# Kernel tuning notes

Measured on AMD Instinct MI355X. Metric: run time of the kernel, lower is better.

The kernel has to match this reference:

```python
import jax, jax.numpy as jnp
import numpy as np

N = 20000      # nodes
E = 320000     # edges (avg degree 16)
IN = 512       # input feature dim
HID = 64       # hidden_dim
NH = 8         # n_heads
NC = 20        # n_classes
NG = 64        # graphs in batch
EPS = 1e-5     # batchnorm eps


def setup_inputs() -> dict:
    key = jax.random.key(0)
    ks = jax.random.split(key, 32)
    rn = lambda k, shape, s=0.05: (jax.random.normal(k, shape, jnp.float32) * s)
    inp = {
        "x": rn(ks[0], (N, IN), 1.0),
        "src": jax.random.randint(ks[1], (E,), 0, N),
        "dst": jax.random.randint(ks[2], (E,), 0, N),
        "graph_ids": jnp.sort(jax.random.randint(ks[3], (N,), 0, NG)),
        "n_graphs": NG,
        # encoder
        "W_enc": rn(ks[4], (IN, HID)), "b_enc": jnp.zeros((HID,), jnp.float32),
        # GAT layer 0
        "fc_W0": rn(ks[5], (HID, NH * HID)),
        "attn_l0": rn(ks[6], (NH, HID)), "attn_r0": rn(ks[7], (NH, HID)),
        "res_W0": rn(ks[8], (HID, NH * HID)),
        "bias0": jnp.zeros((NH * HID,), jnp.float32),
        "dp_W0": rn(ks[9], (NH * HID, HID)), "dp_b0": jnp.zeros((HID,), jnp.float32),
        # GAT layer 1
        "fc_W1": rn(ks[10], (HID, NH * HID)),
        "attn_l1": rn(ks[11], (NH, HID)), "attn_r1": rn(ks[12], (NH, HID)),
        "res_W1": rn(ks[13], (HID, NH * HID)),
        "bias1": jnp.zeros((NH * HID,), jnp.float32),
        "dp_W1": rn(ks[14], (NH * HID, HID)), "dp_b1": jnp.zeros((HID,), jnp.float32),
        # batchnorm affine
        "gamma": jnp.ones((2 * HID,), jnp.float32), "beta": jnp.zeros((2 * HID,), jnp.float32),
        # global attention pooling gate
        "gate_W": rn(ks[15], (2 * HID, 1)), "gate_b": jnp.zeros((1,), jnp.float32),
        # classifier
        "cls_W": rn(ks[16], (2 * HID, NC)), "cls_b": jnp.zeros((NC,), jnp.float32),
    }
    return inp


def gat_conv(h, fc_W, attn_l, attn_r, res_W, bias, src, dst, n_nodes):
    # DGL GATConv: fc -> per-head scalar scores -> edge softmax over incoming
    # edges -> weighted sum -> residual + bias -> leaky_relu activation.
    nh, d = attn_l.shape
    feat = (h @ fc_W).reshape(n_nodes, nh, d)              # [N,H,D]
    el = jnp.sum(feat * attn_l[None], axis=-1)             # [N,H]
    er = jnp.sum(feat * attn_r[None], axis=-1)             # [N,H]
    e = jax.nn.leaky_relu(el[src] + er[dst], 0.2)          # [E,H]
    m = jax.ops.segment_max(e, dst, num_segments=n_nodes)  # segment softmax
    ex = jnp.exp(e - m[dst])
    denom = jax.ops.segment_sum(ex, dst, num_segments=n_nodes)
    a = ex / denom[dst]                                    # [E,H]
    msg = feat[src] * a[:, :, None]                        # [E,H,D]  (dominant)
    rst = jax.ops.segment_sum(msg, dst, num_segments=n_nodes)  # [N,H,D]
    rst = rst + (h @ res_W).reshape(n_nodes, nh, d) + bias.reshape(nh, d)
    return jax.nn.leaky_relu(rst, 0.01)  # F.leaky_relu default slope


def reference(x, W_enc, b_enc,
              fc_W0, attn_l0, attn_r0, res_W0, bias0, dp_W0, dp_b0,
              fc_W1, attn_l1, attn_r1, res_W1, bias1, dp_W1, dp_b1,
              gamma, beta, gate_W, gate_b, cls_W, cls_b,
              src, dst, graph_ids, n_graphs):
    n_nodes = x.shape[0]
    he = x @ W_enc + b_enc                                  # encoder [N,HID]
    h = he
    h = gat_conv(h, fc_W0, attn_l0, attn_r0, res_W0, bias0, src, dst, n_nodes)
    h = h.reshape(n_nodes, -1) @ dp_W0 + dp_b0              # down_proj 0
    h = gat_conv(h, fc_W1, attn_l1, attn_r1, res_W1, bias1, src, dst, n_nodes)
    h = h.reshape(n_nodes, -1) @ dp_W1 + dp_b1              # down_proj 1
    hg = jnp.concatenate([h, he], axis=1)                   # [N,2*HID]
    # BatchNorm1d (training-mode batch stats, biased variance)
    mu = jnp.mean(hg, axis=0)
    var = jnp.var(hg, axis=0)
    hg = (hg - mu) * jax.lax.rsqrt(var + EPS) * gamma + beta
    # GlobalAttentionPooling: per-graph softmax over node gates
    gate = hg @ gate_W + gate_b                             # [N,1]
    gm = jax.ops.segment_max(gate, graph_ids, num_segments=n_graphs)
    ge = jnp.exp(gate - gm[graph_ids])
    gden = jax.ops.segment_sum(ge, graph_ids, num_segments=n_graphs)
    alpha = ge / gden[graph_ids]                            # [N,1]
    readout = jax.ops.segment_sum(alpha * hg, graph_ids, num_segments=n_graphs)
    return readout @ cls_W + cls_b                          # [NG,NC]
```

## Files before the change

### kernel.cpp

```cpp
#include <hip/hip_runtime.h>
#include <hip/hip_bf16.h>

#define MROWS   20000
#define N_EDGES 320000
#define DIN     512
#define HID     64
#define NH      8
#define ND      512
#define NCLS    20
#define NG      64
#define BN_EPS  1e-5f
#define PCH     16
#define BNB     256

typedef __hip_bfloat16 bf16;
typedef __attribute__((ext_vector_type(8))) short s16x8;
typedef __attribute__((ext_vector_type(4))) float f32x4;

enum { TF32 = 0, TBF16 = 1, TMODE = 2 };

__device__ __forceinline__ float ld_f32(const void* p, size_t i) { return ((const float*)p)[i]; }
__device__ __forceinline__ float ld_b16(const void* p, size_t i) { return __bfloat162float(((const bf16*)p)[i]); }

template<int T>
__device__ __forceinline__ float ldT(const void* p, size_t i, int bf) {
    if constexpr (T == TF32) return ld_f32(p, i);
    else if constexpr (T == TBF16) return ld_b16(p, i);
    else return bf ? ld_b16(p, i) : ld_f32(p, i);
}
template<int T>
__device__ __forceinline__ void stT(void* p, size_t i, int bf, float v) {
    if constexpr (T == TF32) ((float*)p)[i] = v;
    else if constexpr (T == TBF16) ((bf16*)p)[i] = __float2bfloat16(v);
    else { if (bf) ((bf16*)p)[i] = __float2bfloat16(v); else ((float*)p)[i] = v; }
}

__device__ __forceinline__ float bfbits2f(short s) {
    return __uint_as_float(((unsigned)(unsigned short)s) << 16);
}
__device__ __forceinline__ short f2bfbits(float v) {
    bf16 b = __float2bfloat16(v);
    return *reinterpret_cast<short*>(&b);
}

__global__ void detect_kernel(const void* __restrict__ gamma, int* __restrict__ mode) {
    if (threadIdx.x == 0 && blockIdx.x == 0)
        *mode = (*(const unsigned*)gamma == 0x3F800000u) ? 0 : 1;
}

struct TP { const void* src[7]; bf16* dst[7]; int K[7]; };
__global__ void transpose7_kernel(TP tp, const int* __restrict__ modep) {
    const int bf = *modep;
    int id = blockIdx.y;
    int i = blockIdx.x * 256 + threadIdx.x;
    int K = tp.K[id];
    int N = (DIN * HID) / K;
    int n = i / K, k = i - n * K;
    tp.dst[id][i] = __float2bfloat16(ldT<TMODE>(tp.src[id], (size_t)k * N + n, bf));
}

__global__ void convx_kernel(const void* __restrict__ x, bf16* __restrict__ xb,
                             const int* __restrict__ modep) {
    if (*modep) return;
    int i = (blockIdx.x * 256 + threadIdx.x) * 4;
    if (i >= MROWS * DIN) return;
    float4 v = ((const float4*)x)[i >> 2];
    xb[i + 0] = __float2bfloat16(v.x);
    xb[i + 1] = __float2bfloat16(v.y);
    xb[i + 2] = __float2bfloat16(v.z);
    xb[i + 3] = __float2bfloat16(v.w);
}

__global__ void hist_kernel(const int* __restrict__ keys, int* __restrict__ counts, int n) {
    int i = blockIdx.x * 256 + threadIdx.x;
    if (i < n) atomicAdd(&counts[keys[i]], 1);
}

__global__ void gsearch_kernel(const int* __restrict__ gids, int* __restrict__ goffs) {
    int g = threadIdx.x;
    if (g > NG) return;
    int lo = 0, hi = MROWS;
    while (lo < hi) {
        int mid = (lo + hi) >> 1;
        if (gids[mid] < g) lo = mid + 1; else hi = mid;
    }
    goffs[g] = lo;
}

__global__ __launch_bounds__(1024)
void scan1_kernel(const int* __restrict__ in, int* __restrict__ out,
                  int* __restrict__ partial, int n) {
    int i = blockIdx.x * 1024 + threadIdx.x;
    int v = (i < n) ? in[i] : 0;
    int lane = threadIdx.x & 63, wid = threadIdx.x >> 6;
    int s = v;
    #pragma unroll
    for (int o = 1; o < 64; o <<= 1) { int t = __shfl_up(s, o, 64); if (lane >= o) s += t; }
    __shared__ int wsum[16];
    if (lane == 63) wsum[wid] = s;
    __syncthreads();
    if (wid == 0 && lane < 16) {
        int t = wsum[lane];
        #pragma unroll
        for (int o = 1; o < 16; o <<= 1) { int u = __shfl_up(t, o, 64); if (lane >= o) t += u; }
        wsum[lane] = t;
    }
    __syncthreads();
    int carry = (wid > 0) ? wsum[wid - 1] : 0;
    int incl = s + carry;
    if (i < n) out[i] = incl - v;
    if (threadIdx.x == 1023) partial[blockIdx.x] = incl;
}

__global__ void scan2_kernel(int* __restrict__ partial, int nb) {
    int l = threadIdx.x;
    int v = (l < nb) ? partial[l] : 0;
    int s = v;
    #pragma unroll
    for (int o = 1; o < 64; o <<= 1) { int t = __shfl_up(s, o, 64); if (l >= o) s += t; }
    if (l < nb) partial[l] = s - v;
}

__global__ __launch_bounds__(1024)
void scan3_kernel(int* __restrict__ out, const int* __restrict__ partial, int n, int total) {
    int i = blockIdx.x * 1024 + threadIdx.x;
    if (i < n) out[i] += partial[blockIdx.x];
    if (i == 0) out[n] = total;
}

__global__ void scatter_kernel(const int* __restrict__ src, const int* __restrict__ dst,
                               const int* __restrict__ offs, int* __restrict__ cursor,
                               int* __restrict__ src_sorted) {
    int e = blockIdx.x * 256 + threadIdx.x;
    if (e < N_EDGES) {
        int d = dst[e];
        int pos = offs[d] + atomicAdd(&cursor[d], 1);
        src_sorted[pos] = src[e];
    }
}

template<int K, int NB, int NTOT>
__global__ __launch_bounds__(256)
void gemm_mfma(const void* __restrict__ Araw, const bf16* __restrict__ Aconv,
               const bf16* __restrict__ BT, const void* __restrict__ bias,
               bf16* __restrict__ C, const int* __restrict__ modep) {
    const int bf = *modep;
    const bf16* A = bf ? (const bf16*)Araw : Aconv;
    const int wid  = threadIdx.x >> 6;
    const int lane = threadIdx.x & 63;
    const int quad = lane >> 4;
    const int l16  = lane & 15;
    const int rb = blockIdx.x * 128 + wid * 32;
    const int cb = blockIdx.y * NB;
    constexpr int CT = NB / 16;
    constexpr int KC = K / 32;

    f32x4 acc[2][CT] = {};
    int r0 = rb + l16;       if (r0 >= MROWS) r0 = MROWS - 1;
    int r1 = rb + 16 + l16;  if (r1 >= MROWS) r1 = MROWS - 1;
    const bf16* a0p = A + (size_t)r0 * K + quad * 8;
    const bf16* a1p = A + (size_t)r1 * K + quad * 8;
    const bf16* btp = BT + (size_t)(cb + l16) * K + quad * 8;

    for (int kc = 0; kc < KC; ++kc) {
        s16x8 af0 = *(const s16x8*)(a0p + kc * 32);
        s16x8 af1 = *(const s16x8*)(a1p + kc * 32);
        s16x8 bfr[CT];
        #pragma unroll
        for (int ct = 0; ct < CT; ++ct)
            bfr[ct] = *(const s16x8*)(btp + (size_t)ct * 16 * K + kc * 32);
        #pragma unroll
        for (int ct = 0; ct < CT; ++ct) {
            acc[0][ct] = __builtin_amdgcn_mfma_f32_16x16x32_bf16(af0, bfr[ct], acc[0][ct], 0, 0, 0);
            acc[1][ct] = __builtin_amdgcn_mfma_f32_16x16x32_bf16(af1, bfr[ct], acc[1][ct], 0, 0, 0);
        }
    }
    #pragma unroll
    for (int ct = 0; ct < CT; ++ct) {
        int col = cb + ct * 16 + l16;
        float bb = bias ? ldT<TMODE>(bias, col, bf) : 0.f;
        #pragma unroll
        for (int rt = 0; rt < 2; ++rt) {
            #pragma unroll
            for (int rg = 0; rg < 4; ++rg) {
                int row = rb + rt * 16 + quad * 4 + rg;
                if (row < MROWS)
                    C[(size_t)row * NTOT + col] = __float2bfloat16(acc[rt][ct][rg] + bb);
            }
        }
    }
}

__global__ __launch_bounds__(256)
void gemm_fcres(const bf16* __restrict__ A, const bf16* __restrict__ BT_fc,
                const bf16* __restrict__ BT_res, const void* __restrict__ bias,
                const void* __restrict__ attn_l, const void* __restrict__ attn_r,
                bf16* __restrict__ feat, bf16* __restrict__ rst,
                float* __restrict__ el, float* __restrict__ er,
                const int* __restrict__ modep) {
    const int bf = *modep;
    const bool isres = blockIdx.y >= 4;
    const int yy = blockIdx.y & 3;
    const bf16* BT = isres ? BT_res : BT_fc;
    bf16* C = isres ? rst : feat;
    const int wid  = threadIdx.x >> 6;
    const int lane = threadIdx.x & 63;
    const int quad = lane >> 4;
    const int l16  = lane & 15;
    const int rb = blockIdx.x * 128 + wid * 32;
    const int cb = yy * 128;
    constexpr int CT = 8;
    constexpr int K  = HID;
    constexpr int KC = K / 32;

    f32x4 acc[2][CT] = {};
    int r0 = rb + l16;       if (r0 >= MROWS) r0 = MROWS - 1;
    int r1 = rb + 16 + l16;  if (r1 >= MROWS) r1 = MROWS - 1;
    const bf16* a0p = A + (size_t)r0 * K + quad * 8;
    const bf16* a1p = A + (size_t)r1 * K + quad * 8;
    const bf16* btp = BT + (size_t)(cb + l16) * K + quad * 8;

    #pragma unroll
    for (int kc = 0; kc < KC; ++kc) {
        s16x8 af0 = *(const s16x8*)(a0p + kc * 32);
        s16x8 af1 = *(const s16x8*)(a1p + kc * 32);
        s16x8 bfr[CT];
        #pragma unroll
        for (int ct = 0; ct < CT; ++ct)
            bfr[ct] = *(const s16x8*)(btp + (size_t)ct * 16 * K + kc * 32);
        #pragma unroll
        for (int ct = 0; ct < CT; ++ct) {
            acc[0][ct] = __builtin_amdgcn_mfma_f32_16x16x32_bf16(af0, bfr[ct], acc[0][ct], 0, 0, 0);
            acc[1][ct] = __builtin_amdgcn_mfma_f32_16x16x32_bf16(af1, bfr[ct], acc[1][ct], 0, 0, 0);
        }
    }
    #pragma unroll
    for (int ct = 0; ct < CT; ++ct) {
        int col = cb + ct * 16 + l16;
        float bb = isres ? ldT<TMODE>(bias, col, bf) : 0.f;
        #pragma unroll
        for (int rt = 0; rt < 2; ++rt) {
            #pragma unroll
            for (int rg = 0; rg < 4; ++rg) {
                int row = rb + rt * 16 + quad * 4 + rg;
                if (row < MROWS)
                    C[(size_t)row * ND + col] = __float2bfloat16(acc[rt][ct][rg] + bb);
            }
        }
    }
    if (!isres) {
        float al[CT], ar[CT];
        #pragma unroll
        for (int ct = 0; ct < CT; ++ct) {
            int col = cb + ct * 16 + l16;
            al[ct] = ldT<TMODE>(attn_l, col, bf);
            ar[ct] = ldT<TMODE>(attn_r, col, bf);
        }
        #pragma unroll
        for (int rt = 0; rt < 2; ++rt) {
            #pragma unroll
            for (int rg = 0; rg < 4; ++rg) {
                float e0 = 0.f, e1 = 0.f, f0 = 0.f, f1 = 0.f;
                #pragma unroll
                for (int ct = 0; ct < 4; ++ct) {
                    e0 += acc[rt][ct][rg] * al[ct];
                    f0 += acc[rt][ct][rg] * ar[ct];
                    e1 += acc[rt][ct + 4][rg] * al[ct + 4];
                    f1 += acc[rt][ct + 4][rg] * ar[ct + 4];
                }
                #pragma unroll
                for (int o = 1; o < 16; o <<= 1) {
                    e0 += __shfl_xor(e0, o, 64);
                    e1 += __shfl_xor(e1, o, 64);
                    f0 += __shfl_xor(f0, o, 64);
                    f1 += __shfl_xor(f1, o, 64);
                }
                int row = rb + rt * 16 + quad * 4 + rg;
                if (row < MROWS) {
                    if (l16 == 0) { el[row * 8 + 2 * yy] = e0;     er[row * 8 + 2 * yy] = f0; }
                    if (l16 == 1) { el[row * 8 + 2 * yy + 1] = e1; er[row * 8 + 2 * yy + 1] = f1; }
                }
            }
        }
    }
}

__global__ __launch_bounds__(256)
void agg_kernel(const bf16* __restrict__ feat, const float* __restrict__ el,
                const float* __restrict__ er, const int* __restrict__ offs,
                const int* __restrict__ srcs, bf16* __restrict__ rst) {
    int gid = blockIdx.x * 256 + threadIdx.x;
    int n = gid >> 6;
    int l = threadIdx.x & 63;
    if (n >= MROWS) return;
    int hh = l >> 3;
    int e0 = __builtin_amdgcn_readfirstlane(offs[n]);
    int e1 = __builtin_amdgcn_readfirstlane(offs[n + 1]);
    float er_h = er[n * 8 + hh];
    float acc[8] = {0.f, 0.f, 0.f, 0.f, 0.f, 0.f, 0.f, 0.f};
    float den = 0.f;
    for (int base = e0; base < e1; base += 64) {
        int cnt = min(64, e1 - base);
        int sv = (base + l < e1) ? srcs[base + l] : 0;
        for (int eb = 0; eb < cnt; eb += 8) {
            int en = cnt - eb;
            s16x8 ff[8];
            float elv[8];
            int lastv = cnt - 1;
            #pragma unroll
            for (int p = 0; p < 8; ++p) {
                int idx = eb + p; if (idx > lastv) idx = lastv;
                int s = __shfl(sv, idx, 64);
                ff[p] = *(const s16x8*)(feat + (size_t)s * ND + l * 8);
                elv[p] = el[s * 8 + hh];
            }
            float ww[8];
            #pragma unroll
            for (int p = 0; p < 8; ++p) {
                float sc = elv[p] + er_h;
                sc = sc > 0.f ? sc : 0.2f * sc;
                ww[p] = __expf(fminf(sc, 30.f));
            }
            if (en < 8) {
                #pragma unroll
                for (int p = 1; p < 8; ++p)
                    if (p >= en) ww[p] = 0.f;
            }
            #pragma unroll
            for (int p = 0; p < 8; ++p) {
                den += ww[p];
                #pragma unroll
                for (int j = 0; j < 8; ++j)
                    acc[j] += bfbits2f(ff[p][j]) * ww[p];
            }
        }
    }
    float inv = (den > 0.f) ? 1.f / den : 0.f;
    s16x8* rp = (s16x8*)(rst + (size_t)n * ND + l * 8);
    s16x8 rr = *rp;
    s16x8 ro;
    #pragma unroll
    for (int j = 0; j < 8; ++j) {
        float r = bfbits2f(rr[j]) + acc[j] * inv;
        r = r > 0.f ? r : 0.01f * r;
        ro[j] = f2bfbits(r);
    }
    *rp = ro;
}

__global__ void bn_part_kernel(const bf16* __restrict__ h2, const bf16* __restrict__ he,
                               float* __restrict__ psum, float* __restrict__ psq) {
    int t = threadIdx.x;
    int b = blockIdx.x;
    int beg = (int)((long)MROWS * b / BNB);
    int end = (int)((long)MROWS * (b + 1) / BNB);
    const bf16* srcb = (t < 64) ? h2 : he;
    int col = t & 63;
    float s = 0.f, s2 = 0.f;
    for (int r = beg; r < end; ++r) {
        float v = __bfloat162float(srcb[(size_t)r * 64 + col]);
        s += v;
        s2 += v * v;
    }
    psum[b * 128 + t] = s;
    psq[b * 128 + t] = s2;
}

__global__ void bn_reduce_kernel(const float* __restrict__ psum, const float* __restrict__ psq,
                                 const void* __restrict__ gamma, const void* __restrict__ beta,
                                 float* __restrict__ scale, float* __restrict__ shift,
                                 const int* __restrict__ modep) {
    const int bf = *modep;
    int t = threadIdx.x;
    float s = 0.f, s2 = 0.f;
    for (int b = 0; b < BNB; ++b) { s += psum[b * 128 + t]; s2 += psq[b * 128 + t]; }
    float mu = s * (1.f / MROWS);
    float var = s2 * (1.f / MROWS) - mu * mu;
    float inv = rsqrtf(fmaxf(var, 0.f) + BN_EPS);
    float a = ldT<TMODE>(gamma, t, bf) * inv;
    scale[t] = a;
    shift[t] = ldT<TMODE>(beta, t, bf) - mu * a;
}

__global__ __launch_bounds__(256)
void gate_kernel(const bf16* __restrict__ h2, const bf16* __restrict__ he,
                 const float* __restrict__ scale, const float* __restrict__ shift,
                 const void* __restrict__ gate_W, const void* __restrict__ gate_b,
                 float* __restrict__ ge, const int* __restrict__ modep) {
    const int bf = *modep;
    int gid = blockIdx.x * 256 + threadIdx.x;
    int r = gid >> 6;
    int l = threadIdx.x & 63;
    if (r >= MROWS) return;
    float v0 = __bfloat162float(h2[(size_t)r * 64 + l]) * scale[l] + shift[l];
    float v1 = __bfloat162float(he[(size_t)r * 64 + l]) * scale[64 + l] + shift[64 + l];
    float s = v0 * ldT<TMODE>(gate_W, l, bf) + v1 * ldT<TMODE>(gate_W, 64 + l, bf);
    #pragma unroll
    for (int o = 32; o > 0; o >>= 1) s += __shfl_xor(s, o, 64);
    if (l == 0) {
        float g = s + ldT<TMODE>(gate_b, 0, bf);
        ge[r] = __expf(fminf(fmaxf(g, -60.f), 30.f));
    }
}

__global__ void pool1_kernel(const bf16* __restrict__ h2, const bf16* __restrict__ he,
                             const float* __restrict__ scale, const float* __restrict__ shift,
                             const float* __restrict__ ge, const int* __restrict__ goffs,
                             float* __restrict__ pacc, float* __restrict__ pden) {
    int g = blockIdx.x;
    int c = blockIdx.y;
    int t = threadIdx.x;
    int r0 = goffs[g], r1 = goffs[g + 1];
    int len = r1 - r0;
    int beg = r0 + (int)((long)len * c / PCH);
    int end = r0 + (int)((long)len * (c + 1) / PCH);
    const bf16* srcb = (t < 64) ? h2 : he;
    int col = t & 63;
    float sc = scale[t], sh = shift[t];
    float acc = 0.f, den = 0.f;
    for (int r = beg; r < end; ++r) {
        float wg = ge[r];
        float v = __bfloat162float(srcb[(size_t)r * 64 + col]) * sc + sh;
        den += wg;
        acc += wg * v;
    }
    pacc[((size_t)g * PCH + c) * 128 + t] = acc;
    if (t == 0) pden[g * PCH + c] = den;
}

__global__ void pool2_kernel(const float* __restrict__ pacc, const float* __restrict__ pden,
                             float* __restrict__ readout) {
    int g = blockIdx.x;
    int t = threadIdx.x;
    float acc = 0.f, den = 0.f;
    #pragma unroll
    for (int c = 0; c < PCH; ++c) {
        acc += pacc[((size_t)g * PCH + c) * 128 + t];
        den += pden[g * PCH + c];
    }
    readout[g * 128 + t] = (den > 0.f) ? acc / den : 0.f;
}

__global__ void cls_kernel(const float* __restrict__ readout, const void* __restrict__ W,
                           const void* __restrict__ b, void* __restrict__ out,
                           const int* __restrict__ modep) {
    const int bf = *modep;
    int i = blockIdx.x * 256 + threadIdx.x;
    if (i >= NG * NCLS) return;
    int g = i / NCLS, c = i - g * NCLS;
    float acc = ldT<TMODE>(b, c, bf);
    #pragma unroll 8
    for (int k = 0; k < 128; ++k)
        acc += readout[g * 128 + k] * ldT<TMODE>(W, k * NCLS + c, bf);
    stT<TMODE>(out, i, bf, acc);
}

extern "C" void kernel_launch(void* const* d_in, const int* in_sizes, int n_in,
                              void* d_out, int out_size, void* d_ws, size_t ws_size,
                              hipStream_t stream) {
    const void* x       = d_in[0];
    const int*  src     = (const int*)d_in[1];
    const int*  dst     = (const int*)d_in[2];
    const int*  gids    = (const int*)d_in[3];
    const void* W_enc   = d_in[5];
    const void* b_enc   = d_in[6];
    const void* fc_W0   = d_in[7];
    const void* attn_l0 = d_in[8];
    const void* attn_r0 = d_in[9];
    const void* res_W0  = d_in[10];
    const void* bias0   = d_in[11];
    const void* dp_W0   = d_in[12];
    const void* dp_b0   = d_in[13];
    const void* fc_W1   = d_in[14];
    const void* attn_l1 = d_in[15];
    const void* attn_r1 = d_in[16];
    const void* res_W1  = d_in[17];
    const void* bias1   = d_in[18];
    const void* dp_W1   = d_in[19];
    const void* dp_b1   = d_in[20];
    const void* gamma   = d_in[21];
    const void* beta    = d_in[22];
    const void* gate_W  = d_in[23];
    const void* gate_b  = d_in[24];
    const void* cls_W   = d_in[25];
    const void* cls_b   = d_in[26];

    char* wsc = (char*)d_ws;
    size_t off = 0;
    auto alloc = [&](size_t bytes) -> void* {
        void* p = wsc + off;
        off = (off + bytes + 255) & ~(size_t)255;
        return p;
    };
    bf16*  he        = (bf16*) alloc((size_t)MROWS * HID * 2);
    bf16*  h         = (bf16*) alloc((size_t)MROWS * HID * 2);
    bf16*  h2        = (bf16*) alloc((size_t)MROWS * HID * 2);
    bf16*  feat      = (bf16*) alloc((size_t)MROWS * ND * 2);
    bf16*  rst       = (bf16*) alloc((size_t)MROWS * ND * 2);
    bf16*  xb        = rst;
    bf16*  bt_enc    = (bf16*) alloc((size_t)DIN * HID * 2);
    bf16*  bt_fc0    = (bf16*) alloc((size_t)HID * ND * 2);
    bf16*  bt_res0   = (bf16*) alloc((size_t)HID * ND * 2);
    bf16*  bt_dp0    = (bf16*) alloc((size_t)ND * HID * 2);
    bf16*  bt_fc1    = (bf16*) alloc((size_t)HID * ND * 2);
    bf16*  bt_res1   = (bf16*) alloc((size_t)HID * ND * 2);
    bf16*  bt_dp1    = (bf16*) alloc((size_t)ND * HID * 2);
    float* el        = (float*)alloc((size_t)MROWS * 8 * 4);
    float* er        = (float*)alloc((size_t)MROWS * 8 * 4);
    float* ge        = (float*)alloc((size_t)MROWS * 4);
    float* readout   = (float*)alloc((size_t)NG * 128 * 4);
    int*   src_sorted= (int*)  alloc((size_t)N_EDGES * 4);
    int*   offs      = (int*)  alloc((size_t)(MROWS + 1) * 4);
    int*   goffs     = (int*)  alloc((size_t)(NG + 1) * 4);
    int*   spartial  = (int*)  alloc(64 * 4);
    float* psum      = (float*)alloc((size_t)BNB * 128 * 4);
    float* psq       = (float*)alloc((size_t)BNB * 128 * 4);
    float* pacc      = (float*)alloc((size_t)NG * PCH * 128 * 4);
    float* pden      = (float*)alloc((size_t)NG * PCH * 4);
    float* bnscale   = (float*)alloc(128 * 4);
    float* bnshift   = (float*)alloc(128 * 4);
    int*   mode      = (int*)  alloc(4);
    size_t zbytes = (size_t)MROWS * 4 * 2;
    char*  zbase  = (char*)alloc(zbytes);
    int* counts  = (int*)zbase;
    int* cursor  = counts + MROWS;

    hipMemsetAsync(zbase, 0, zbytes, stream);
    detect_kernel<<<1, 64, 0, stream>>>(gamma, mode);

    TP tp;
    tp.src[0] = W_enc;  tp.K[0] = DIN;
    tp.src[1] = fc_W0;  tp.K[1] = HID;
    tp.src[2] = res_W0; tp.K[2] = HID;
    tp.src[3] = dp_W0;  tp.K[3] = ND;
    tp.src[4] = fc_W1;  tp.K[4] = HID;
    tp.src[5] = res_W1; tp.K[5] = HID;
    tp.src[6] = dp_W1;  tp.K[6] = ND;
    tp.dst[0] = bt_enc; tp.dst[1] = bt_fc0; tp.dst[2] = bt_res0; tp.dst[3] = bt_dp0;
    tp.dst[4] = bt_fc1; tp.dst[5] = bt_res1; tp.dst[6] = bt_dp1;
    transpose7_kernel<<<dim3((DIN * HID) / 256, 7), 256, 0, stream>>>(tp, mode);
    convx_kernel<<<(MROWS * DIN / 4 + 255) / 256, 256, 0, stream>>>(x, xb, mode);

    hist_kernel<<<(N_EDGES + 255) / 256, 256, 0, stream>>>(dst, counts, N_EDGES);
    gsearch_kernel<<<1, 128, 0, stream>>>(gids, goffs);
    const int SB = (MROWS + 1023) / 1024;
    scan1_kernel<<<SB, 1024, 0, stream>>>(counts, offs, spartial, MROWS);
    scan2_kernel<<<1, 64, 0, stream>>>(spartial, SB);
    scan3_kernel<<<SB, 1024, 0, stream>>>(offs, spartial, MROWS, N_EDGES);
    scatter_kernel<<<(N_EDGES + 255) / 256, 256, 0, stream>>>(src, dst, offs, cursor, src_sorted);

    const int GX = (MROWS + 127) / 128;

    gemm_mfma<DIN, 64, 64><<<dim3(GX, 1), 256, 0, stream>>>(x, xb, bt_enc, b_enc, he, mode);

    gemm_fcres<<<dim3(GX, 8), 256, 0, stream>>>(he, bt_fc0, bt_res0, bias0, attn_l0, attn_r0,
                                                feat, rst, el, er, mode);
    agg_kernel<<<(MROWS * 64) / 256, 256, 0, stream>>>(feat, el, er, offs, src_sorted, rst);
    gemm_mfma<ND, 64, 64><<<dim3(GX, 1), 256, 0, stream>>>(rst, rst, bt_dp0, dp_b0, h, mode);

    gemm_fcres<<<dim3(GX, 8), 256, 0, stream>>>(h, bt_fc1, bt_res1, bias1, attn_l1, attn_r1,
                                                feat, rst, el, er, mode);
    agg_kernel<<<(MROWS * 64) / 256, 256, 0, stream>>>(feat, el, er, offs, src_sorted, rst);
    gemm_mfma<ND, 64, 64><<<dim3(GX, 1), 256, 0, stream>>>(rst, rst, bt_dp1, dp_b1, h2, mode);

    bn_part_kernel<<<BNB, 128, 0, stream>>>(h2, he, psum, psq);
    bn_reduce_kernel<<<1, 128, 0, stream>>>(psum, psq, gamma, beta, bnscale, bnshift, mode);
    gate_kernel<<<(MROWS * 64 + 255) / 256, 256, 0, stream>>>(h2, he, bnscale, bnshift, gate_W, gate_b, ge, mode);
    pool1_kernel<<<dim3(NG, PCH), 128, 0, stream>>>(h2, he, bnscale, bnshift, ge, goffs, pacc, pden);
    pool2_kernel<<<NG, 128, 0, stream>>>(pacc, pden, readout);
    cls_kernel<<<(NG * NCLS + 255) / 256, 256, 0, stream>>>(readout, cls_W, cls_b, d_out, mode);
}
```

Measured before the change: 471.6 us.

## Merge small prep, scan, gate and classifier kernels to cut launch count

Removes the mode-detect kernel by having each kernel check gamma inline, and replaces the memset with zeroing inside one prep kernel that also does the weight transposes and the x conversion. The three-pass scan and the graph-offset search become one single-block kernel. The gate computation moves into the pooling loop, and pool2 is fused with the classifier. The aim is less launch overhead, but the single-block scan is serial and the fused pool loop adds two block barriers per node row, which may lengthen those stages.

After: 478.5 us. About the same (+1.5%).

```diff
diff --git a/kernel.cpp b/kernel.cpp
--- a/kernel.cpp
+++ b/kernel.cpp
@@ -12,12 +12,17 @@
 #define BN_EPS  1e-5f
 #define PCH     16
 #define BNB     256
+#define TPB     128
 
 typedef __hip_bfloat16 bf16;
 typedef __attribute__((ext_vector_type(8))) short s16x8;
 typedef __attribute__((ext_vector_type(4))) float f32x4;
 
 enum { TF32 = 0, TBF16 = 1, TMODE = 2 };
+
+__device__ __forceinline__ int is_bf16_mode(const void* gamma) {
+    return *(const unsigned*)gamma != 0x3F800000u;
+}
 
 __device__ __forceinline__ float ld_f32(const void* p, size_t i) { return ((const float*)p)[i]; }
 __device__ __forceinline__ float ld_b16(const void* p, size_t i) { return __bfloat162float(((const bf16*)p)[i]); }
@@ -43,32 +48,30 @@
     return *reinterpret_cast<short*>(&b);
 }
 
-__global__ void detect_kernel(const void* __restrict__ gamma, int* __restrict__ mode) {
-    if (threadIdx.x == 0 && blockIdx.x == 0)
-        *mode = (*(const unsigned*)gamma == 0x3F800000u) ? 0 : 1;
-}
-
 struct TP { const void* src[7]; bf16* dst[7]; int K[7]; };
-__global__ void transpose7_kernel(TP tp, const int* __restrict__ modep) {
-    const int bf = *modep;
-    int id = blockIdx.y;
-    int i = blockIdx.x * 256 + threadIdx.x;
-    int K = tp.K[id];
-    int N = (DIN * HID) / K;
-    int n = i / K, k = i - n * K;
-    tp.dst[id][i] = __float2bfloat16(ldT<TMODE>(tp.src[id], (size_t)k * N + n, bf));
-}
-
-__global__ void convx_kernel(const void* __restrict__ x, bf16* __restrict__ xb,
-                             const int* __restrict__ modep) {
-    if (*modep) return;
-    int i = (blockIdx.x * 256 + threadIdx.x) * 4;
-    if (i >= MROWS * DIN) return;
-    float4 v = ((const float4*)x)[i >> 2];
-    xb[i + 0] = __float2bfloat16(v.x);
-    xb[i + 1] = __float2bfloat16(v.y);
-    xb[i + 2] = __float2bfloat16(v.z);
-    xb[i + 3] = __float2bfloat16(v.w);
+__global__ void prep_kernel(TP tp, const void* __restrict__ x, bf16* __restrict__ xb,
+                            const void* __restrict__ gamma, int* __restrict__ zero0) {
+    int b = blockIdx.x;
+    int z = b * 256 + threadIdx.x;
+    if (z < 2 * MROWS) zero0[z] = 0;
+    const int bf = is_bf16_mode(gamma);
+    if (b < 7 * TPB) {
+        int id = b / TPB;
+        int i = (b - id * TPB) * 256 + threadIdx.x;
+        int K = tp.K[id];
+        int N = (DIN * HID) / K;
+        int n = i / K, k = i - n * K;
+        tp.dst[id][i] = __float2bfloat16(ldT<TMODE>(tp.src[id], (size_t)k * N + n, bf));
+    } else {
+        if (bf) return;
+        int i = ((b - 7 * TPB) * 256 + threadIdx.x) * 4;
+        if (i >= MROWS * DIN) return;
+        float4 v = ((const float4*)x)[i >> 2];
+        xb[i + 0] = __float2bfloat16(v.x);
+        xb[i + 1] = __float2bfloat16(v.y);
+        xb[i + 2] = __float2bfloat16(v.z);
+        xb[i + 3] = __float2bfloat16(v.w);
+    }
 }
 
 __global__ void hist_kernel(const int* __restrict__ keys, int* __restrict__ counts, int n) {
@@ -76,56 +79,46 @@
     if (i < n) atomicAdd(&counts[keys[i]], 1);
 }
 
-__global__ void gsearch_kernel(const int* __restrict__ gids, int* __restrict__ goffs) {
-    int g = threadIdx.x;
-    if (g > NG) return;
-    int lo = 0, hi = MROWS;
-    while (lo < hi) {
-        int mid = (lo + hi) >> 1;
-        if (gids[mid] < g) lo = mid + 1; else hi = mid;
-    }
-    goffs[g] = lo;
-}
-
 __global__ __launch_bounds__(1024)
-void scan1_kernel(const int* __restrict__ in, int* __restrict__ out,
-                  int* __restrict__ partial, int n) {
-    int i = blockIdx.x * 1024 + threadIdx.x;
-    int v = (i < n) ? in[i] : 0;
+void scan_all_kernel(const int* __restrict__ counts, int* __restrict__ offs,
+                     const int* __restrict__ gids, int* __restrict__ goffs) {
+    if (threadIdx.x <= NG) {
+        int g = threadIdx.x;
+        int lo = 0, hi = MROWS;
+        while (lo < hi) {
+            int mid = (lo + hi) >> 1;
+            if (gids[mid] < g) lo = mid + 1; else hi = mid;
+        }
+        goffs[g] = lo;
+    }
+    __shared__ int wsum[16];
+    __shared__ int carry_s;
+    int carry = 0;
     int lane = threadIdx.x & 63, wid = threadIdx.x >> 6;
-    int s = v;
-    #pragma unroll
-    for (int o = 1; o < 64; o <<= 1) { int t = __shfl_up(s, o, 64); if (lane >= o) s += t; }
-    __shared__ int wsum[16];
-    if (lane == 63) wsum[wid] = s;
-    __syncthreads();
-    if (wid == 0 && lane < 16) {
-        int t = wsum[lane];
-        #pragma unroll
-        for (int o = 1; o < 16; o <<= 1) { int u = __shfl_up(t, o, 64); if (lane >= o) t += u; }
-        wsum[lane] = t;
-    }
-    __syncthreads();
-    int carry = (wid > 0) ? wsum[wid - 1] : 0;
-    int incl = s + carry;
-    if (i < n) out[i] = incl - v;
-    if (threadIdx.x == 1023) partial[blockIdx.x] = incl;
-}
-
-__global__ void scan2_kernel(int* __restrict__ partial, int nb) {
-    int l = threadIdx.x;
-    int v = (l < nb) ? partial[l] : 0;
-    int s = v;
-    #pragma unroll
-    for (int o = 1; o < 64; o <<= 1) { int t = __shfl_up(s, o, 64); if (l >= o) s += t; }
-    if (l < nb) partial[l] = s - v;
-}
-
-__global__ __launch_bounds__(1024)
-void scan3_kernel(int* __restrict__ out, const int* __restrict__ partial, int n, int total) {
-    int i = blockIdx.x * 1024 + threadIdx.x;
-    if (i < n) out[i] += partial[blockIdx.x];
-    if (i == 0) out[n] = total;
+    const int NCHUNK = (MROWS + 1023) / 1024;
+    for (int ch = 0; ch < NCHUNK; ++ch) {
+        int i = ch * 1024 + threadIdx.x;
+        int v = (i < MROWS) ? counts[i] : 0;
+        int s = v;
+        #pragma unroll
+        for (int o = 1; o < 64; o <<= 1) { int t = __shfl_up(s, o, 64); if (lane >= o) s += t; }
+        if (lane == 63) wsum[wid] = s;
+        __syncthreads();
+        if (wid == 0 && lane < 16) {
+            int t = wsum[lane];
+            #pragma unroll
+            for (int o = 1; o < 16; o <<= 1) { int u = __shfl_up(t, o, 64); if (lane >= o) t += u; }
+            wsum[lane] = t;
+        }
+        __syncthreads();
+        int wc = (wid > 0) ? wsum[wid - 1] : 0;
+        int incl = s + wc + carry;
+        if (i < MROWS) offs[i] = incl - v;
+        if (threadIdx.x == 1023) carry_s = incl;
+        __syncthreads();
+        carry = carry_s;
+    }
+    if (threadIdx.x == 0) offs[MROWS] = carry;
 }
 
 __global__ void scatter_kernel(const int* __restrict__ src, const int* __restrict__ dst,
@@ -143,8 +136,8 @@
 __global__ __launch_bounds__(256)
 void gemm_mfma(const void* __restrict__ Araw, const bf16* __restrict__ Aconv,
                const bf16* __restrict__ BT, const void* __restrict__ bias,
-               bf16* __restrict__ C, const int* __restrict__ modep) {
-    const int bf = *modep;
+               bf16* __restrict__ C, const void* __restrict__ gamma) {
+    const int bf = is_bf16_mode(gamma);
     const bf16* A = bf ? (const bf16*)Araw : Aconv;
     const int wid  = threadIdx.x >> 6;
     const int lane = threadIdx.x & 63;
@@ -197,8 +190,8 @@
                 const void* __restrict__ attn_l, const void* __restrict__ attn_r,
                 bf16* __restrict__ feat, bf16* __restrict__ rst,
                 float* __restrict__ el, float* __restrict__ er,
-                const int* __restrict__ modep) {
-    const int bf = *modep;
+                const void* __restrict__ gamma) {
+    const int bf = is_bf16_mode(gamma);
     const bool isres = blockIdx.y >= 4;
     const int yy = blockIdx.y & 3;
     const bf16* BT = isres ? BT_res : BT_fc;
@@ -368,9 +361,8 @@
 
 __global__ void bn_reduce_kernel(const float* __restrict__ psum, const float* __restrict__ psq,
                                  const void* __restrict__ gamma, const void* __restrict__ beta,
-                                 float* __restrict__ scale, float* __restrict__ shift,
-                                 const int* __restrict__ modep) {
-    const int bf = *modep;
+                                 float* __restrict__ scale, float* __restrict__ shift) {
+    const int bf = is_bf16_mode(gamma);
     int t = threadIdx.x;
     float s = 0.f, s2 = 0.f;
     for (int b = 0; b < BNB; ++b) { s += psum[b * 128 + t]; s2 += psq[b * 128 + t]; }
@@ -382,31 +374,14 @@
     shift[t] = ldT<TMODE>(beta, t, bf) - mu * a;
 }
 
-__global__ __launch_bounds__(256)
-void gate_kernel(const bf16* __restrict__ h2, const bf16* __restrict__ he,
-                 const float* __restrict__ scale, const float* __restrict__ shift,
-                 const void* __restrict__ gate_W, const void* __restrict__ gate_b,
-                 float* __restrict__ ge, const int* __restrict__ modep) {
-    const int bf = *modep;
-    int gid = blockIdx.x * 256 + threadIdx.x;
-    int r = gid >> 6;
-    int l = threadIdx.x & 63;
-    if (r >= MROWS) return;
-    float v0 = __bfloat162float(h2[(size_t)r * 64 + l]) * scale[l] + shift[l];
-    float v1 = __bfloat162float(he[(size_t)r * 64 + l]) * scale[64 + l] + shift[64 + l];
-    float s = v0 * ldT<TMODE>(gate_W, l, bf) + v1 * ldT<TMODE>(gate_W, 64 + l, bf);
-    #pragma unroll
-    for (int o = 32; o > 0; o >>= 1) s += __shfl_xor(s, o, 64);
-    if (l == 0) {
-        float g = s + ldT<TMODE>(gate_b, 0, bf);
-        ge[r] = __expf(fminf(fmaxf(g, -60.f), 30.f));
-    }
-}
-
-__global__ void pool1_kernel(const bf16* __restrict__ h2, const bf16* __restrict__ he,
-                             const float* __restrict__ scale, const float* __restrict__ shift,
-                             const float* __restrict__ ge, const int* __restrict__ goffs,
-                             float* __restrict__ pacc, float* __restrict__ pden) {
+__global__ __launch_bounds__(128)
+void poolgate_kernel(const bf16* __restrict__ h2, const bf16* __restrict__ he,
+                     const float* __restrict__ scale, const float* __restrict__ shift,
+                     const void* __restrict__ gate_W, const void* __restrict__ gate_b,
+                     const int* __restrict__ goffs,
+                     float* __restrict__ pacc, float* __restrict__ pden,
+                     const void* __restrict__ gamma) {
+    const int bf = is_bf16_mode(gamma);
     int g = blockIdx.x;
     int c = blockIdx.y;
     int t = threadIdx.x;
@@ -417,19 +392,31 @@
     const bf16* srcb = (t < 64) ? h2 : he;
     int col = t & 63;
     float sc = scale[t], sh = shift[t];
+    float gw = ldT<TMODE>(gate_W, t, bf);
+    float gb = ldT<TMODE>(gate_b, 0, bf);
+    __shared__ float ws[2];
     float acc = 0.f, den = 0.f;
     for (int r = beg; r < end; ++r) {
-        float wg = ge[r];
         float v = __bfloat162float(srcb[(size_t)r * 64 + col]) * sc + sh;
+        float p = v * gw;
+        #pragma unroll
+        for (int o = 32; o > 0; o >>= 1) p += __shfl_xor(p, o, 64);
+        if ((t & 63) == 0) ws[t >> 6] = p;
+        __syncthreads();
+        float wg = __expf(fminf(fmaxf(ws[0] + ws[1] + gb, -60.f), 30.f));
         den += wg;
         acc += wg * v;
+        __syncthreads();
     }
     pacc[((size_t)g * PCH + c) * 128 + t] = acc;
     if (t == 0) pden[g * PCH + c] = den;
 }
 
-__global__ void pool2_kernel(const float* __restrict__ pacc, const float* __restrict__ pden,
-                             float* __restrict__ readout) {
+__global__ __launch_bounds__(128)
+void poolcls_kernel(const float* __restrict__ pacc, const float* __restrict__ pden,
+                    const void* __restrict__ W, const void* __restrict__ b,
+                    void* __restrict__ out, const void* __restrict__ gamma) {
+    const int bf = is_bf16_mode(gamma);
     int g = blockIdx.x;
     int t = threadIdx.x;
     float acc = 0.f, den = 0.f;
@@ -438,21 +425,16 @@
         acc += pacc[((size_t)g * PCH + c) * 128 + t];
         den += pden[g * PCH + c];
     }
-    readout[g * 128 + t] = (den > 0.f) ? acc / den : 0.f;
-}
-
-__global__ void cls_kernel(const float* __restrict__ readout, const void* __restrict__ W,
-                           const void* __restrict__ b, void* __restrict__ out,
-                           const int* __restrict__ modep) {
-    const int bf = *modep;
-    int i = blockIdx.x * 256 + threadIdx.x;
-    if (i >= NG * NCLS) return;
-    int g = i / NCLS, c = i - g * NCLS;
-    float acc = ldT<TMODE>(b, c, bf);
-    #pragma unroll 8
-    for (int k = 0; k < 128; ++k)
-        acc += readout[g * 128 + k] * ldT<TMODE>(W, k * NCLS + c, bf);
-    stT<TMODE>(out, i, bf, acc);
+    __shared__ float rs[128];
+    rs[t] = (den > 0.f) ? acc / den : 0.f;
+    __syncthreads();
+    if (t < NCLS) {
+        float o = ldT<TMODE>(b, t, bf);
+        #pragma unroll 8
+        for (int k = 0; k < 128; ++k)
+            o += rs[k] * ldT<TMODE>(W, (size_t)k * NCLS + t, bf);
+        stT<TMODE>(out, g * NCLS + t, bf, o);
+    }
 }
 
 extern "C" void kernel_launch(void* const* d_in, const int* in_sizes, int n_in,
@@ -507,26 +489,18 @@
     bf16*  bt_dp1    = (bf16*) alloc((size_t)ND * HID * 2);
     float* el        = (float*)alloc((size_t)MROWS * 8 * 4);
     float* er        = (float*)alloc((size_t)MROWS * 8 * 4);
-    float* ge        = (float*)alloc((size_t)MROWS * 4);
-    float* readout   = (float*)alloc((size_t)NG * 128 * 4);
     int*   src_sorted= (int*)  alloc((size_t)N_EDGES * 4);
     int*   offs      = (int*)  alloc((size_t)(MROWS + 1) * 4);
     int*   goffs     = (int*)  alloc((size_t)(NG + 1) * 4);
-    int*   spartial  = (int*)  alloc(64 * 4);
     float* psum      = (float*)alloc((size_t)BNB * 128 * 4);
     float* psq       = (float*)alloc((size_t)BNB * 128 * 4);
     float* pacc      = (float*)alloc((size_t)NG * PCH * 128 * 4);
     float* pden      = (float*)alloc((size_t)NG * PCH * 4);
     float* bnscale   = (float*)alloc(128 * 4);
     float* bnshift   = (float*)alloc(128 * 4);
-    int*   mode      = (int*)  alloc(4);
-    size_t zbytes = (size_t)MROWS * 4 * 2;
-    char*  zbase  = (char*)alloc(zbytes);
+    char*  zbase     = (char*) alloc((size_t)MROWS * 4 * 2);
     int* counts  = (int*)zbase;
     int* cursor  = counts + MROWS;
-
-    hipMemsetAsync(zbase, 0, zbytes, stream);
-    detect_kernel<<<1, 64, 0, stream>>>(gamma, mode);
 
     TP tp;
     tp.src[0] = W_enc;  tp.K[0] = DIN;
@@ -538,35 +512,30 @@
     tp.src[6] = dp_W1;  tp.K[6] = ND;
     tp.dst[0] = bt_enc; tp.dst[1] = bt_fc0; tp.dst[2] = bt_res0; tp.dst[3] = bt_dp0;
     tp.dst[4] = bt_fc1; tp.dst[5] = bt_res1; tp.dst[6] = bt_dp1;
-    transpose7_kernel<<<dim3((DIN * HID) / 256, 7), 256, 0, stream>>>(tp, mode);
-    convx_kernel<<<(MROWS * DIN / 4 + 255) / 256, 256, 0, stream>>>(x, xb, mode);
+    const int CONVB = (MROWS * DIN / 4) / 256;
+    prep_kernel<<<7 * TPB + CONVB, 256, 0, stream>>>(tp, x, xb, gamma, (int*)zbase);
 
     hist_kernel<<<(N_EDGES + 255) / 256, 256, 0, stream>>>(dst, counts, N_EDGES);
-    gsearch_kernel<<<1, 128, 0, stream>>>(gids, goffs);
-    const int SB = (MROWS + 1023) / 1024;
-    scan1_kernel<<<SB, 1024, 0, stream>>>(counts, offs, spartial, MROWS);
-    scan2_kernel<<<1, 64, 0, stream>>>(spartial, SB);
-    scan3_kernel<<<SB, 1024, 0, stream>>>(offs, spartial, MROWS, N_EDGES);
+    scan_all_kernel<<<1, 1024, 0, stream>>>(counts, offs, gids, goffs);
     scatter_kernel<<<(N_EDGES + 255) / 256, 256, 0, stream>>>(src, dst, offs, cursor, src_sorted);
 
     const int GX = (MROWS + 127) / 128;
 
-    gemm_mfma<DIN, 64, 64><<<dim3(GX, 1), 256, 0, stream>>>(x, xb, bt_enc, b_enc, he, mode);
+    gemm_mfma<DIN, 64, 64><<<dim3(GX, 1), 256, 0, stream>>>(x, xb, bt_enc, b_enc, he, gamma);
 
     gemm_fcres<<<dim3(GX, 8), 256, 0, stream>>>(he, bt_fc0, bt_res0, bias0, attn_l0, attn_r0,
-                                                feat, rst, el, er, mode);
+                                                feat, rst, el, er, gamma);
     agg_kernel<<<(MROWS * 64) / 256, 256, 0, stream>>>(feat, el, er, offs, src_sorted, rst);
-    gemm_mfma<ND, 64, 64><<<dim3(GX, 1), 256, 0, stream>>>(rst, rst, bt_dp0, dp_b0, h, mode);
+    gemm_mfma<ND, 64, 64><<<dim3(GX, 1), 256, 0, stream>>>(rst, rst, bt_dp0, dp_b0, h, gamma);
 
     gemm_fcres<<<dim3(GX, 8), 256, 0, stream>>>(h, bt_fc1, bt_res1, bias1, attn_l1, attn_r1,
-                                                feat, rst, el, er, mode);
+                                                feat, rst, el, er, gamma);
     agg_kernel<<<(MROWS * 64) / 256, 256, 0, stream>>>(feat, el, er, offs, src_sorted, rst);
-    gemm_mfma<ND, 64, 64><<<dim3(GX, 1), 256, 0, stream>>>(rst, rst, bt_dp1, dp_b1, h2, mode);
+    gemm_mfma<ND, 64, 64><<<dim3(GX, 1), 256, 0, stream>>>(rst, rst, bt_dp1, dp_b1, h2, gamma);
 
     bn_part_kernel<<<BNB, 128, 0, stream>>>(h2, he, psum, psq);
-    bn_reduce_kernel<<<1, 128, 0, stream>>>(psum, psq, gamma, beta, bnscale, bnshift, mode);
-    gate_kernel<<<(MROWS * 64 + 255) / 256, 256, 0, stream>>>(h2, he, bnscale, bnshift, gate_W, gate_b, ge, mode);
-    pool1_kernel<<<dim3(NG, PCH), 128, 0, stream>>>(h2, he, bnscale, bnshift, ge, goffs, pacc, pden);
-    pool2_kernel<<<NG, 128, 0, stream>>>(pacc, pden, readout);
-    cls_kernel<<<(NG * NCLS + 255) / 256, 256, 0, stream>>>(readout, cls_W, cls_b, d_out, mode);
-}
+    bn_reduce_kernel<<<1, 128, 0, stream>>>(psum, psq, gamma, beta, bnscale, bnshift);
+    poolgate_kernel<<<dim3(NG, PCH), 128, 0, stream>>>(h2, he, bnscale, bnshift, gate_W, gate_b,
+                                                       goffs, pacc, pden, gamma);
+    poolcls_kernel<<<NG, 128, 0, stream>>>(pacc, pden, cls_W, cls_b, d_out, gamma);
+}
```
